# Performance work log

Hardware: AMD Instinct MI355X
Metric: run time of the kernel (lower is better)

## Reference

```python
import jax, jax.numpy as jnp
import numpy as np

ALPHA = 0.2  # leaky relu negative slope


def setup_inputs() -> dict:
    key = jax.random.key(0)
    ks = jax.random.split(key, 6)
    B, K, F = 8, 256, 64
    E = 2 * F  # gatv2 embed dim
    x = jax.random.normal(ks[0], (B, K, F), dtype=jnp.float32)
    lin_w = jax.random.normal(ks[1], (E, 2 * F), dtype=jnp.float32) * 0.05
    lin_b = jax.random.normal(ks[2], (E,), dtype=jnp.float32) * 0.05
    a = jax.random.normal(ks[3], (E, 1), dtype=jnp.float32) * 0.05
    att_bias = jnp.zeros((K, K), dtype=jnp.float32)
    fc_w = jax.random.normal(ks[4], (64, F), dtype=jnp.float32) * 0.05
    fc_b = jax.random.normal(ks[5], (64,), dtype=jnp.float32) * 0.05
    return {"x": x, "lin_w": lin_w, "lin_b": lin_b, "a": a,
            "att_bias": att_bias, "fc_w": fc_w, "fc_b": fc_b}


def reference(x, lin_w, lin_b, a, att_bias, fc_w, fc_b):
    # GATv2 temporal attention. Original builds a_input[b,i,j] = concat(x[b,i], x[b,j])
    # then lin(a_input). Since lin is linear, decompose W = [W1 | W2] so that
    # lin(concat(xi, xj)) = xi @ W1^T + xj @ W2^T + b  -- identical math,
    # avoids the [B,K,K,2F] concat tensor.
    F_dim = x.shape[-1]
    w1 = lin_w[:, :F_dim]   # [E, F] applied to the repeated (i) block
    w2 = lin_w[:, F_dim:]   # [E, F] applied to the alternating (j) block
    s_i = jnp.einsum('bkf,ef->bke', x, w1)           # [B,K,E]
    s_j = jnp.einsum('bkf,ef->bke', x, w2)           # [B,K,E]
    hidden = s_i[:, :, None, :] + s_j[:, None, :, :] + lin_b  # [B,K,K,E]
    hidden = jnp.where(hidden >= 0, hidden, ALPHA * hidden)   # leaky relu
    e = jnp.einsum('bije,e->bij', hidden, a[:, 0])            # [B,K,K]
    e = e + att_bias                                           # bias [K,K]
    attention = jax.nn.softmax(e, axis=2)
    # dropout p=0.0 -> identity
    h = jax.nn.sigmoid(jnp.einsum('bij,bjf->bif', attention, x))  # [B,K,F]
    return jnp.einsum('bkf,of->bko', h, fc_w) + fc_b              # [B,K,out_dim]
```

## Files before the change

### kernel.cpp

```cpp
#include <hip/hip_runtime.h>
#include <hip/hip_bf16.h>

#define ALPHA 0.2f
constexpr int B = 8, K = 256, F = 64, E = 128;


__device__ __forceinline__ float term4(float4 aa, float4 uu, float4 vv, float acc) {
    acc = fmaf(aa.x, fabsf(uu.x + vv.x), acc);
    acc = fmaf(aa.y, fabsf(uu.y + vv.y), acc);
    acc = fmaf(aa.z, fabsf(uu.z + vv.z), acc);
    acc = fmaf(aa.w, fabsf(uu.w + vv.w), acc);
    return acc;
}

__global__ __launch_bounds__(256) void gat_kA(
    const float* __restrict__ x, const float* __restrict__ lin_w,
    const float* __restrict__ lin_b, const float* __restrict__ a,
    const float* __restrict__ fc_w,
    float* __restrict__ u, float* __restrict__ vT,
    float* __restrict__ c, float* __restrict__ d,
    float4* __restrict__ fcp)
{
    const int t = threadIdx.x;
    const int wave = t >> 6, lane = t & 63;
    const int row0 = blockIdx.x * 8;
    const int e = t & 127, rh = t >> 7;
    const int b = row0 >> 8;

    __shared__ float4 wls[4096];
    __shared__ alignas(16) float xs[8 * F];
    __shared__ float redA[4][8];

    const float4* lw4 = (const float4*)lin_w;
#pragma unroll
    for (int i = 0; i < 16; ++i) {
        int idx = i * 256 + t;
        int ee = idx >> 5, cc = idx & 31;
        wls[(ee << 5) | (cc ^ (ee & 31))] = lw4[idx];
    }
    xs[t]       = x[row0 * F + t];
    xs[t + 256] = x[row0 * F + t + 256];

    if (blockIdx.x == 0) {
#pragma unroll
        for (int i = 0; i < 4; ++i) {
            int k = i * 256 + t;
            int f4 = k >> 6, o = k & 63;
            const float* r = fc_w + o * F + f4 * 4;
            fcp[k] = make_float4(r[0], r[1], r[2], r[3]);
        }
    }
    __syncthreads();

    const int ebase = e << 5, ex = e & 31;
    float acc1[4] = {0, 0, 0, 0}, acc2[4] = {0, 0, 0, 0};
#pragma unroll
    for (int p = 0; p < 16; ++p) {
        float4 w1 = wls[ebase + (p ^ ex)];
        float4 w2 = wls[ebase + ((16 | p) ^ ex)];
#pragma unroll
        for (int r = 0; r < 4; ++r) {
            float4 xv = *(const float4*)&xs[(rh * 4 + r) * F + 4 * p];
            acc1[r] = fmaf(w1.x, xv.x, acc1[r]); acc1[r] = fmaf(w1.y, xv.y, acc1[r]);
            acc1[r] = fmaf(w1.z, xv.z, acc1[r]); acc1[r] = fmaf(w1.w, xv.w, acc1[r]);
            acc2[r] = fmaf(w2.x, xv.x, acc2[r]); acc2[r] = fmaf(w2.y, xv.y, acc2[r]);
            acc2[r] = fmaf(w2.z, xv.z, acc2[r]); acc2[r] = fmaf(w2.w, xv.w, acc2[r]);
        }
    }
    const float bb = lin_b[e], av = a[e];
    float vals[8];
#pragma unroll
    for (int r = 0; r < 4; ++r) {
        const float uu = acc1[r] + bb;
        const int rr = row0 + rh * 4 + r;
        u[rr * E + e] = uu;
        vT[((b * 32 + (e >> 2)) * K + (rr & (K - 1))) * 4 + (e & 3)] = acc2[r];
        vals[r * 2 + 0] = av * acc2[r];
        vals[r * 2 + 1] = av * uu;
    }
#pragma unroll
    for (int off = 32; off; off >>= 1) {
#pragma unroll
        for (int q = 0; q < 8; ++q) vals[q] += __shfl_xor(vals[q], off);
    }
    if (lane == 0) {
#pragma unroll
        for (int q = 0; q < 8; ++q) redA[wave][q] = vals[q];
    }
    __syncthreads();
    if (t < 16) {
        const int half = t >> 3, loc = t & 7;
        const int r = loc >> 1, cd = loc & 1;
        float val = redA[2 * half][loc] + redA[2 * half + 1][loc];
        const int row = row0 + half * 4 + r;
        if (cd == 0) c[row] = val; else d[row] = val;
    }
}

__global__ __launch_bounds__(512) void gat_kB(
    const float* __restrict__ x, const float* __restrict__ a,
    const float* __restrict__ att_bias, const float4* __restrict__ fcp,
    const float* __restrict__ fc_b, const float* __restrict__ u,
    const float4* __restrict__ vT4, const float* __restrict__ c,
    const float* __restrict__ d, float* __restrict__ out)
{
    const int blk = blockIdx.x;
    const int b = blk >> 5;
    const int i0 = (blk & 31) * 8;
    const int t = threadIdx.x;
    const int wave = t >> 6, lane = t & 63;

    __shared__ float part[8][8][K];
    __shared__ float ps[8][K];
    __shared__ float4 hpart[8][8][16];
    __shared__ float4 h4s[8][16];

    {
        const int jj = lane;
        const float4* v4  = vT4 + (size_t)b * 32 * K + (size_t)wave * 4 * K + jj;
        const float4* u4g = (const float4*)(u + (size_t)(b * K + i0) * E);
        const float4* a4g = (const float4*)a;
        float ej[8][4];
#pragma unroll
        for (int i = 0; i < 8; ++i)
#pragma unroll
            for (int q = 0; q < 4; ++q) ej[i][q] = 0.f;

#pragma unroll
        for (int it = 0; it < 4; ++it) {
            const int e4 = wave * 4 + it;
            float4 aa = a4g[e4];
            float4 vv0 = v4[it * K + 0 * 64];
            float4 vv1 = v4[it * K + 1 * 64];
            float4 vv2 = v4[it * K + 2 * 64];
            float4 vv3 = v4[it * K + 3 * 64];
#pragma unroll
            for (int i = 0; i < 8; ++i) {
                float4 uu = u4g[i * 32 + e4];
                ej[i][0] = term4(aa, uu, vv0, ej[i][0]);
                ej[i][1] = term4(aa, uu, vv1, ej[i][1]);
                ej[i][2] = term4(aa, uu, vv2, ej[i][2]);
                ej[i][3] = term4(aa, uu, vv3, ej[i][3]);
            }
        }
#pragma unroll
        for (int i = 0; i < 8; ++i)
#pragma unroll
            for (int q = 0; q < 4; ++q)
                part[wave][i][q * 64 + jj] = ej[i][q];
    }
    __syncthreads();

    {
        const int w = wave;
        const float dw = d[b * K + i0 + w];
        float ex[4], ssum = 0.f;
#pragma unroll
        for (int q = 0; q < 4; ++q) {
            const int j = q * 64 + lane;
            float s = part[0][w][j] + part[1][w][j] + part[2][w][j] + part[3][w][j]
                    + part[4][w][j] + part[5][w][j] + part[6][w][j] + part[7][w][j];
            float cv = c[b * K + j];
            float av = att_bias[(i0 + w) * K + j];
            float e  = fmaf(0.4f, s, fmaf(0.6f, dw + cv, av));
            ex[q] = __expf(e);
            ssum += ex[q];
        }
#pragma unroll
        for (int off = 32; off; off >>= 1) ssum += __shfl_xor(ssum, off);
        const float inv = 1.f / ssum;
#pragma unroll
        for (int q = 0; q < 4; ++q) ps[w][q * 64 + lane] = ex[q] * inv;
    }
    __syncthreads();

    {
        const int jg = t >> 4, fq = t & 15;
        const float4* xb4 = (const float4*)x + (size_t)b * K * 16 + fq;
        const float4* ps4 = (const float4*)ps;
        float4 h[8];
#pragma unroll
        for (int i = 0; i < 8; ++i) h[i] = make_float4(0, 0, 0, 0);
#pragma unroll
        for (int m = 0; m < 2; ++m) {
            const int j = jg * 8 + m * 4;
            float4 xa = xb4[(size_t)(j + 0) * 16];
            float4 xb = xb4[(size_t)(j + 1) * 16];
            float4 xc = xb4[(size_t)(j + 2) * 16];
            float4 xd = xb4[(size_t)(j + 3) * 16];
#pragma unroll
            for (int i = 0; i < 8; ++i) {
                float4 p = ps4[i * 64 + jg * 2 + m];
                h[i].x = fmaf(p.x, xa.x, h[i].x); h[i].y = fmaf(p.x, xa.y, h[i].y);
                h[i].z = fmaf(p.x, xa.z, h[i].z); h[i].w = fmaf(p.x, xa.w, h[i].w);
                h[i].x = fmaf(p.y, xb.x, h[i].x); h[i].y = fmaf(p.y, xb.y, h[i].y);
                h[i].z = fmaf(p.y, xb.z, h[i].z); h[i].w = fmaf(p.y, xb.w, h[i].w);
                h[i].x = fmaf(p.z, xc.x, h[i].x); h[i].y = fmaf(p.z, xc.y, h[i].y);
                h[i].z = fmaf(p.z, xc.z, h[i].z); h[i].w = fmaf(p.z, xc.w, h[i].w);
                h[i].x = fmaf(p.w, xd.x, h[i].x); h[i].y = fmaf(p.w, xd.y, h[i].y);
                h[i].z = fmaf(p.w, xd.z, h[i].z); h[i].w = fmaf(p.w, xd.w, h[i].w);
            }
        }
#pragma unroll
        for (int off = 16; off <= 32; off <<= 1) {
#pragma unroll
            for (int i = 0; i < 8; ++i) {
                h[i].x += __shfl_xor(h[i].x, off); h[i].y += __shfl_xor(h[i].y, off);
                h[i].z += __shfl_xor(h[i].z, off); h[i].w += __shfl_xor(h[i].w, off);
            }
        }
        if (lane < 16) {
#pragma unroll
            for (int i = 0; i < 8; ++i) hpart[wave][i][lane] = h[i];
        }
    }
    __syncthreads();
    if (t < 128) {
        const int i = t >> 4, f4 = t & 15;
        float4 hv = make_float4(0, 0, 0, 0);
#pragma unroll
        for (int w = 0; w < 8; ++w) {
            float4 A = hpart[w][i][f4];
            hv.x += A.x; hv.y += A.y; hv.z += A.z; hv.w += A.w;
        }
        hv.x = 1.f / (1.f + __expf(-hv.x)); hv.y = 1.f / (1.f + __expf(-hv.y));
        hv.z = 1.f / (1.f + __expf(-hv.z)); hv.w = 1.f / (1.f + __expf(-hv.w));
        h4s[i][f4] = hv;
    }
    __syncthreads();

    {
        float acc = 0.f;
#pragma unroll
        for (int f4 = 0; f4 < 16; ++f4) {
            float4 hv = h4s[wave][f4];
            float4 wv = fcp[f4 * 64 + lane];
            acc = fmaf(hv.x, wv.x, acc); acc = fmaf(hv.y, wv.y, acc);
            acc = fmaf(hv.z, wv.z, acc); acc = fmaf(hv.w, wv.w, acc);
        }
        out[(b * K + i0 + wave) * F + lane] = acc + fc_b[lane];
    }
}

extern "C" void kernel_launch(void* const* d_in, const int* in_sizes, int n_in,
                              void* d_out, int out_size, void* d_ws, size_t ws_size,
                              hipStream_t stream) {
    const float* x        = (const float*)d_in[0];
    const float* lin_w    = (const float*)d_in[1];
    const float* lin_b    = (const float*)d_in[2];
    const float* a        = (const float*)d_in[3];
    const float* att_bias = (const float*)d_in[4];
    const float* fc_w     = (const float*)d_in[5];
    const float* fc_b     = (const float*)d_in[6];
    float* out = (float*)d_out;

    float* u   = (float*)d_ws;
    float* vT  = u + B * K * E;
    float* c   = vT + B * K * E;
    float* d   = c + B * K;
    float4* fcp = (float4*)(d + B * K);

    gat_kA<<<B * K / 8, 256, 0, stream>>>(x, lin_w, lin_b, a, fc_w,
                                          u, vT, c, d, fcp);
    gat_kB<<<B * K / 8, 512, 0, stream>>>(x, a, att_bias, fcp, fc_b, u,
                                          (const float4*)vT, c, d, out);
}
```

Baseline: 21.50 us.

## Store u/v intermediates in fp16 and use packed fdot2 for attention scores

The u and vT intermediates are now written as half precision, which halves workspace traffic between the two kernels. The pairwise |u+v|·a inner loop uses packed half adds, a bit-mask abs and fdot2 accumulation into fp32, with the 0.4 scale folded into a precomputed fp16 copy of a. The first kernel also moves to 512 threads with 2 rows per thread instead of 4. The risk is fp16 rounding in the attention logits, which could push error past tolerance.

```diff
diff --git a/kernel.cpp b/kernel.cpp
--- a/kernel.cpp
+++ b/kernel.cpp
@@ -4,22 +4,31 @@
 #define ALPHA 0.2f
 constexpr int B = 8, K = 256, F = 64, E = 128;
 
-
-__device__ __forceinline__ float term4(float4 aa, float4 uu, float4 vv, float acc) {
-    acc = fmaf(aa.x, fabsf(uu.x + vv.x), acc);
-    acc = fmaf(aa.y, fabsf(uu.y + vv.y), acc);
-    acc = fmaf(aa.z, fabsf(uu.z + vv.z), acc);
-    acc = fmaf(aa.w, fabsf(uu.w + vv.w), acc);
-    return acc;
-}
-
-__global__ __launch_bounds__(256) void gat_kA(
+typedef _Float16 h2 __attribute__((ext_vector_type(2)));
+
+union H4 { uint2 u; struct { h2 lo, hi; } p; };
+
+__device__ __forceinline__ h2 habs2(h2 v) {
+    unsigned x; __builtin_memcpy(&x, &v, 4);
+    x &= 0x7FFF7FFFu;
+    __builtin_memcpy(&v, &x, 4);
+    return v;
+}
+
+#if __has_builtin(__builtin_amdgcn_fdot2)
+#define FDOT2(a, b, c) __builtin_amdgcn_fdot2((a), (b), (c), false)
+#else
+#define FDOT2(a, b, c) ((c) + (float)(a)[0] * (float)(b)[0] + (float)(a)[1] * (float)(b)[1])
+#endif
+
+
+__global__ __launch_bounds__(512) void gat_kA(
     const float* __restrict__ x, const float* __restrict__ lin_w,
     const float* __restrict__ lin_b, const float* __restrict__ a,
     const float* __restrict__ fc_w,
-    float* __restrict__ u, float* __restrict__ vT,
+    _Float16* __restrict__ u_h, _Float16* __restrict__ vT_h,
     float* __restrict__ c, float* __restrict__ d,
-    float4* __restrict__ fcp)
+    float4* __restrict__ fcp, _Float16* __restrict__ a_h)
 {
     const int t = threadIdx.x;
     const int wave = t >> 6, lane = t & 63;
@@ -29,38 +38,38 @@
 
     __shared__ float4 wls[4096];
     __shared__ alignas(16) float xs[8 * F];
-    __shared__ float redA[4][8];
+    __shared__ float redA[8][4];
 
     const float4* lw4 = (const float4*)lin_w;
 #pragma unroll
-    for (int i = 0; i < 16; ++i) {
-        int idx = i * 256 + t;
+    for (int i = 0; i < 8; ++i) {
+        int idx = i * 512 + t;
         int ee = idx >> 5, cc = idx & 31;
         wls[(ee << 5) | (cc ^ (ee & 31))] = lw4[idx];
     }
-    xs[t]       = x[row0 * F + t];
-    xs[t + 256] = x[row0 * F + t + 256];
+    xs[t] = x[row0 * F + t];
 
     if (blockIdx.x == 0) {
 #pragma unroll
-        for (int i = 0; i < 4; ++i) {
-            int k = i * 256 + t;
+        for (int i = 0; i < 2; ++i) {
+            int k = i * 512 + t;
             int f4 = k >> 6, o = k & 63;
             const float* r = fc_w + o * F + f4 * 4;
             fcp[k] = make_float4(r[0], r[1], r[2], r[3]);
         }
+        if (t < 128) a_h[t] = (_Float16)(0.4f * a[t]);
     }
     __syncthreads();
 
     const int ebase = e << 5, ex = e & 31;
-    float acc1[4] = {0, 0, 0, 0}, acc2[4] = {0, 0, 0, 0};
+    float acc1[2] = {0, 0}, acc2[2] = {0, 0};
 #pragma unroll
     for (int p = 0; p < 16; ++p) {
         float4 w1 = wls[ebase + (p ^ ex)];
         float4 w2 = wls[ebase + ((16 | p) ^ ex)];
 #pragma unroll
-        for (int r = 0; r < 4; ++r) {
-            float4 xv = *(const float4*)&xs[(rh * 4 + r) * F + 4 * p];
+        for (int r = 0; r < 2; ++r) {
+            float4 xv = *(const float4*)&xs[(rh * 2 + r) * F + 4 * p];
             acc1[r] = fmaf(w1.x, xv.x, acc1[r]); acc1[r] = fmaf(w1.y, xv.y, acc1[r]);
             acc1[r] = fmaf(w1.z, xv.z, acc1[r]); acc1[r] = fmaf(w1.w, xv.w, acc1[r]);
             acc2[r] = fmaf(w2.x, xv.x, acc2[r]); acc2[r] = fmaf(w2.y, xv.y, acc2[r]);
@@ -68,40 +77,40 @@
         }
     }
     const float bb = lin_b[e], av = a[e];
-    float vals[8];
-#pragma unroll
-    for (int r = 0; r < 4; ++r) {
+    float vals[4];
+#pragma unroll
+    for (int r = 0; r < 2; ++r) {
         const float uu = acc1[r] + bb;
-        const int rr = row0 + rh * 4 + r;
-        u[rr * E + e] = uu;
-        vT[((b * 32 + (e >> 2)) * K + (rr & (K - 1))) * 4 + (e & 3)] = acc2[r];
+        const int rr = row0 + rh * 2 + r;
+        u_h[rr * E + e] = (_Float16)uu;
+        vT_h[(((b * 32) + (e >> 2)) * K + (rr & (K - 1))) * 4 + (e & 3)] =
+            (_Float16)acc2[r];
         vals[r * 2 + 0] = av * acc2[r];
         vals[r * 2 + 1] = av * uu;
     }
 #pragma unroll
     for (int off = 32; off; off >>= 1) {
 #pragma unroll
-        for (int q = 0; q < 8; ++q) vals[q] += __shfl_xor(vals[q], off);
+        for (int q = 0; q < 4; ++q) vals[q] += __shfl_xor(vals[q], off);
     }
     if (lane == 0) {
 #pragma unroll
-        for (int q = 0; q < 8; ++q) redA[wave][q] = vals[q];
+        for (int q = 0; q < 4; ++q) redA[wave][q] = vals[q];
     }
     __syncthreads();
     if (t < 16) {
-        const int half = t >> 3, loc = t & 7;
-        const int r = loc >> 1, cd = loc & 1;
-        float val = redA[2 * half][loc] + redA[2 * half + 1][loc];
-        const int row = row0 + half * 4 + r;
+        const int rh2 = t >> 2, r = (t >> 1) & 1, cd = t & 1;
+        float val = redA[rh2 * 2][r * 2 + cd] + redA[rh2 * 2 + 1][r * 2 + cd];
+        const int row = row0 + rh2 * 2 + r;
         if (cd == 0) c[row] = val; else d[row] = val;
     }
 }
 
 __global__ __launch_bounds__(512) void gat_kB(
-    const float* __restrict__ x, const float* __restrict__ a,
+    const float* __restrict__ x, const _Float16* __restrict__ a_h,
     const float* __restrict__ att_bias, const float4* __restrict__ fcp,
-    const float* __restrict__ fc_b, const float* __restrict__ u,
-    const float4* __restrict__ vT4, const float* __restrict__ c,
+    const float* __restrict__ fc_b, const _Float16* __restrict__ u_h,
+    const uint2* __restrict__ vTh2, const float* __restrict__ c,
     const float* __restrict__ d, float* __restrict__ out)
 {
     const int blk = blockIdx.x;
@@ -117,9 +126,9 @@
 
     {
         const int jj = lane;
-        const float4* v4  = vT4 + (size_t)b * 32 * K + (size_t)wave * 4 * K + jj;
-        const float4* u4g = (const float4*)(u + (size_t)(b * K + i0) * E);
-        const float4* a4g = (const float4*)a;
+        const uint2* v2 = vTh2 + (size_t)b * 32 * K + (size_t)wave * 4 * K + jj;
+        const uint2* u2 = (const uint2*)(u_h + (size_t)(b * K + i0) * E);
+        const uint2* a2 = (const uint2*)a_h;
         float ej[8][4];
 #pragma unroll
         for (int i = 0; i < 8; ++i)
@@ -129,18 +138,35 @@
 #pragma unroll
         for (int it = 0; it < 4; ++it) {
             const int e4 = wave * 4 + it;
-            float4 aa = a4g[e4];
-            float4 vv0 = v4[it * K + 0 * 64];
-            float4 vv1 = v4[it * K + 1 * 64];
-            float4 vv2 = v4[it * K + 2 * 64];
-            float4 vv3 = v4[it * K + 3 * 64];
+            H4 av; av.u = a2[e4];
+            H4 vv0, vv1, vv2, vv3;
+            vv0.u = v2[it * K + 0 * 64];
+            vv1.u = v2[it * K + 1 * 64];
+            vv2.u = v2[it * K + 2 * 64];
+            vv3.u = v2[it * K + 3 * 64];
 #pragma unroll
             for (int i = 0; i < 8; ++i) {
-                float4 uu = u4g[i * 32 + e4];
-                ej[i][0] = term4(aa, uu, vv0, ej[i][0]);
-                ej[i][1] = term4(aa, uu, vv1, ej[i][1]);
-                ej[i][2] = term4(aa, uu, vv2, ej[i][2]);
-                ej[i][3] = term4(aa, uu, vv3, ej[i][3]);
+                H4 uu; uu.u = u2[i * 32 + e4];
+                {
+                    h2 t0 = habs2(uu.p.lo + vv0.p.lo), t1 = habs2(uu.p.hi + vv0.p.hi);
+                    ej[i][0] = FDOT2(av.p.lo, t0, ej[i][0]);
+                    ej[i][0] = FDOT2(av.p.hi, t1, ej[i][0]);
+                }
+                {
+                    h2 t0 = habs2(uu.p.lo + vv1.p.lo), t1 = habs2(uu.p.hi + vv1.p.hi);
+                    ej[i][1] = FDOT2(av.p.lo, t0, ej[i][1]);
+                    ej[i][1] = FDOT2(av.p.hi, t1, ej[i][1]);
+                }
+                {
+                    h2 t0 = habs2(uu.p.lo + vv2.p.lo), t1 = habs2(uu.p.hi + vv2.p.hi);
+                    ej[i][2] = FDOT2(av.p.lo, t0, ej[i][2]);
+                    ej[i][2] = FDOT2(av.p.hi, t1, ej[i][2]);
+                }
+                {
+                    h2 t0 = habs2(uu.p.lo + vv3.p.lo), t1 = habs2(uu.p.hi + vv3.p.hi);
+                    ej[i][3] = FDOT2(av.p.lo, t0, ej[i][3]);
+                    ej[i][3] = FDOT2(av.p.hi, t1, ej[i][3]);
+                }
             }
         }
 #pragma unroll
@@ -162,7 +188,7 @@
                     + part[4][w][j] + part[5][w][j] + part[6][w][j] + part[7][w][j];
             float cv = c[b * K + j];
             float av = att_bias[(i0 + w) * K + j];
-            float e  = fmaf(0.4f, s, fmaf(0.6f, dw + cv, av));
+            float e  = s + fmaf(0.6f, dw + cv, av);
             ex[q] = __expf(e);
             ssum += ex[q];
         }
@@ -254,14 +280,15 @@
     const float* fc_b     = (const float*)d_in[6];
     float* out = (float*)d_out;
 
-    float* u   = (float*)d_ws;
-    float* vT  = u + B * K * E;
-    float* c   = vT + B * K * E;
-    float* d   = c + B * K;
+    _Float16* u_h  = (_Float16*)d_ws;
+    _Float16* vT_h = u_h + B * K * E;
+    float* c = (float*)(vT_h + B * K * E);
+    float* d = c + B * K;
     float4* fcp = (float4*)(d + B * K);
-
-    gat_kA<<<B * K / 8, 256, 0, stream>>>(x, lin_w, lin_b, a, fc_w,
-                                          u, vT, c, d, fcp);
-    gat_kB<<<B * K / 8, 512, 0, stream>>>(x, a, att_bias, fcp, fc_b, u,
-                                          (const float4*)vT, c, d, out);
-}
+    _Float16* a_h = (_Float16*)(fcp + 1024);
+
+    gat_kA<<<B * K / 8, 512, 0, stream>>>(x, lin_w, lin_b, a, fc_w,
+                                          u_h, vT_h, c, d, fcp, a_h);
+    gat_kB<<<B * K / 8, 512, 0, stream>>>(x, a_h, att_bias, fcp, fc_b, u_h,
+                                          (const uint2*)vT_h, c, d, out);
+}
```

Result: faster. 19.66 us (median of 2 runs) (-8.6%).
